# Kernel tuning notes

Hardware: AMD Instinct MI355X
Metric: run time of the kernel (lower is better)

The kernel has to match this reference:

```python
import jax, jax.numpy as jnp
import numpy as np

N_NODES = 100000
N_EDGES = 1600000
IN_CH, HID_CH, N_CLASS = 512, 128, 40


def setup_inputs() -> dict:
    key = jax.random.key(0)
    k1, k2, k3, k4 = jax.random.split(key, 4)
    x = jax.random.normal(k1, (N_NODES, IN_CH), dtype=jnp.float32)
    edge_index = jax.random.randint(k2, (2, N_EDGES), 0, N_NODES, dtype=jnp.int64)
    W1 = jax.random.normal(k3, (IN_CH, HID_CH), dtype=jnp.float32) * (1.0 / np.sqrt(IN_CH))
    b1 = jnp.zeros((HID_CH,), dtype=jnp.float32)
    W2 = jax.random.normal(k4, (HID_CH, N_CLASS), dtype=jnp.float32) * (1.0 / np.sqrt(HID_CH))
    b2 = jnp.zeros((N_CLASS,), dtype=jnp.float32)
    return {"x": x, "edge_index": edge_index, "W1": W1, "b1": b1, "W2": W2, "b2": b2}


def _gcn_conv(x, src, dst, norm, W, b, n_nodes):
    # transform then sparse normalized aggregation: out = D^-1/2 (A+I) D^-1/2 (x W) + b
    h = x @ W                                  # [N, out_ch]
    msg = h[src] * norm[:, None]               # gather + scale, [E+N, out_ch]
    return jax.ops.segment_sum(msg, dst, num_segments=n_nodes) + b


def reference(x, edge_index, W1, b1, W2, b2):
    n = x.shape[0]
    loop = jnp.arange(n, dtype=edge_index.dtype)
    src = jnp.concatenate([edge_index[0], loop])   # add self-loops
    dst = jnp.concatenate([edge_index[1], loop])
    deg = jax.ops.segment_sum(jnp.ones_like(src, dtype=x.dtype), dst, num_segments=n)
    dinv = jnp.where(deg > 0, jax.lax.rsqrt(deg), 0.0)
    norm = dinv[src] * dinv[dst]                   # symmetric normalization

    h = jax.nn.relu(_gcn_conv(x, src, dst, norm, W1, b1, n))
    # dropout(p=0.5, train=False) -> identity in eval mode
    logits = _gcn_conv(h, src, dst, norm, W2, b2, n)
    return jax.nn.log_softmax(logits, axis=1)
```

## Files before the change

kernel.cpp:

```cpp
#include <hip/hip_runtime.h>
#include <math.h>

#define IN_CH 512
#define HID 128
#define NCLASS 40
#define SCAN_CHUNK 2048
#define FILL_CHUNKS 2048

typedef __attribute__((ext_vector_type(8))) short short8;
typedef __attribute__((ext_vector_type(4))) float float4v;

static __device__ inline ushort f2bf(float f) {
    unsigned int u = __float_as_uint(f);
    u += 0x7fffu + ((u >> 16) & 1u);
    return (ushort)(u >> 16);
}
static __device__ inline float bf2f(ushort u) {
    return __uint_as_float(((unsigned int)u) << 16);
}

__global__ void k_count(const int* __restrict__ dst, int E, int* __restrict__ cnt) {
    int i = blockIdx.x * blockDim.x + threadIdx.x;
    if (i < E) atomicAdd(&cnt[dst[i]], 1);
}

__global__ void k_dinv(const int* __restrict__ cnt, float* __restrict__ dinv, int n) {
    int i = blockIdx.x * blockDim.x + threadIdx.x;
    if (i < n) dinv[i] = rsqrtf((float)cnt[i] + 1.0f);
}

__global__ __launch_bounds__(256) void k_scan_local(const int* __restrict__ cnt,
                                                    int* __restrict__ rowptr,
                                                    int* __restrict__ blocksum, int n) {
    __shared__ int ssum[256];
    int b = blockIdx.x, t = threadIdx.x;
    int base = b * SCAN_CHUNK + t * 8;
    int v[8], s = 0;
    #pragma unroll
    for (int i = 0; i < 8; ++i) {
        int idx = base + i;
        v[i] = (idx < n) ? cnt[idx] : 0;
        s += v[i];
    }
    ssum[t] = s;
    __syncthreads();
    for (int off = 1; off < 256; off <<= 1) {
        int x = (t >= off) ? ssum[t - off] : 0;
        __syncthreads();
        ssum[t] += x;
        __syncthreads();
    }
    int run = ssum[t] - s;
    #pragma unroll
    for (int i = 0; i < 8; ++i) {
        int idx = base + i;
        if (idx < n) rowptr[idx] = run;
        run += v[i];
    }
    if (t == 255) blocksum[b] = ssum[255];
}

__global__ void k_scan_blocksums(int* blocksum, int nb) {
    if (threadIdx.x == 0 && blockIdx.x == 0) {
        int acc = 0;
        for (int i = 0; i < nb; ++i) { int v = blocksum[i]; blocksum[i] = acc; acc += v; }
    }
}

__global__ void k_scan_add(int* __restrict__ rowptr, int* __restrict__ cursor,
                           const int* __restrict__ blocksum, int n) {
    int i = blockIdx.x * blockDim.x + threadIdx.x;
    if (i < n) {
        int r = rowptr[i] + blocksum[i / SCAN_CHUNK];
        rowptr[i] = r;
        cursor[i] = r;
    }
}

__global__ __launch_bounds__(256) void k_fill(const int* __restrict__ src,
                                              const int* __restrict__ dst,
                                              int* __restrict__ cursor,
                                              int* __restrict__ col, int E, int N) {
    int range = blockIdx.x & 7;
    int chunk = blockIdx.x >> 3;
    int r0 = (N >> 3) * range;
    int r1 = (range == 7) ? N : r0 + (N >> 3);
    int e0 = (int)((long long)E * chunk / FILL_CHUNKS);
    int e1 = (int)((long long)E * (chunk + 1) / FILL_CHUNKS);
    for (int e = e0 + threadIdx.x; e < e1; e += 256) {
        int d = dst[e];
        if (d >= r0 && d < r1) {
            int p = atomicAdd(&cursor[d], 1);
            col[p] = src[e];
        }
    }
}

__global__ void k_w1t(const float* __restrict__ W1, ushort* __restrict__ W1t) {
    int i = blockIdx.x * blockDim.x + threadIdx.x;
    int n = i >> 9;
    int k = i & 511;
    W1t[i] = f2bf(W1[k * HID + n]);
}

#define GBM 128
#define GBK 64
#define KP 72
__global__ __launch_bounds__(256) void k_gemm1_mfma(const float* __restrict__ X,
                                                    const ushort* __restrict__ W1t,
                                                    ushort* __restrict__ H, int M) {
    __shared__ ushort As[GBM * KP];
    int t = threadIdx.x;
    int bm = blockIdx.x * GBM;
    int wave = t >> 6;
    int lane = t & 63;
    int m0w = (wave >> 1) * 64;
    int n0w = (wave & 1) * 64;
    int lrow = lane & 15;
    int quad = lane >> 4;

    float4v acc[4][4];
    #pragma unroll
    for (int i = 0; i < 4; ++i)
        #pragma unroll
        for (int j = 0; j < 4; ++j) acc[i][j] = (float4v)(0.f);

    int ar = t >> 1;
    int ah = (t & 1) * 32;
    int gmr = bm + ar;
    if (gmr >= M) gmr = M - 1;
    const float* gA = &X[(size_t)gmr * IN_CH + ah];

    float4 pre[8];
    #pragma unroll
    for (int i = 0; i < 8; ++i) pre[i] = *(const float4*)(gA + i * 4);

    for (int k0 = 0; k0 < IN_CH; k0 += GBK) {
        #pragma unroll
        for (int i = 0; i < 4; ++i) {
            union { ushort u[8]; uint4 v; } pk;
            float4 f0 = pre[2 * i], f1 = pre[2 * i + 1];
            pk.u[0] = f2bf(f0.x); pk.u[1] = f2bf(f0.y);
            pk.u[2] = f2bf(f0.z); pk.u[3] = f2bf(f0.w);
            pk.u[4] = f2bf(f1.x); pk.u[5] = f2bf(f1.y);
            pk.u[6] = f2bf(f1.z); pk.u[7] = f2bf(f1.w);
            *(uint4*)&As[ar * KP + ah + i * 8] = pk.v;
        }
        if (k0 + GBK < IN_CH) {
            #pragma unroll
            for (int i = 0; i < 8; ++i)
                pre[i] = *(const float4*)(gA + k0 + GBK + i * 4);
        }
        __syncthreads();
        #pragma unroll
        for (int kk = 0; kk < GBK; kk += 32) {
            short8 af[4], bfr[4];
            #pragma unroll
            for (int j = 0; j < 4; ++j)
                bfr[j] = *(const short8*)&W1t[(size_t)(n0w + j * 16 + lrow) * IN_CH
                                              + k0 + kk + quad * 8];
            #pragma unroll
            for (int i = 0; i < 4; ++i)
                af[i] = *(const short8*)&As[(m0w + i * 16 + lrow) * KP + kk + quad * 8];
            #pragma unroll
            for (int i = 0; i < 4; ++i)
                #pragma unroll
                for (int j = 0; j < 4; ++j)
                    acc[i][j] = __builtin_amdgcn_mfma_f32_16x16x32_bf16(
                        af[i], bfr[j], acc[i][j], 0, 0, 0);
        }
        __syncthreads();
    }
    #pragma unroll
    for (int i = 0; i < 4; ++i) {
        #pragma unroll
        for (int r = 0; r < 4; ++r) {
            int gm = bm + m0w + i * 16 + quad * 4 + r;
            if (gm < M) {
                #pragma unroll
                for (int j = 0; j < 4; ++j)
                    H[(size_t)gm * HID + n0w + j * 16 + lrow] = f2bf(acc[i][j][r]);
            }
        }
    }
}

__global__ __launch_bounds__(256) void k_agg1_gemm2(const int* __restrict__ rowptr,
                                                    const int* __restrict__ rowend,
                                                    const int* __restrict__ col,
                                                    const float* __restrict__ dinv,
                                                    const unsigned int* __restrict__ h1b,
                                                    const float* __restrict__ b1,
                                                    const float* __restrict__ W2,
                                                    unsigned int* __restrict__ h2p, int N) {
    __shared__ float hs[4][HID];
    int wv = threadIdx.x >> 6;
    int t  = threadIdx.x & 63;
    int m = blockIdx.x * 4 + wv;
    if (m >= N) m = N - 1;
    float dm = dinv[m];
    unsigned int sv = h1b[(size_t)m * 64 + t];
    float sw = dm * dm;
    float ax = bf2f((ushort)(sv & 0xffff)) * sw;
    float ay = bf2f((ushort)(sv >> 16)) * sw;
    int j = rowptr[m], jend = rowend[m];
    for (; j + 4 <= jend; j += 4) {
        int s0 = col[j], s1 = col[j + 1], s2 = col[j + 2], s3 = col[j + 3];
        float n0 = dinv[s0] * dm, n1 = dinv[s1] * dm;
        float n2 = dinv[s2] * dm, n3 = dinv[s3] * dm;
        unsigned int v0 = h1b[(size_t)s0 * 64 + t];
        unsigned int v1 = h1b[(size_t)s1 * 64 + t];
        unsigned int v2 = h1b[(size_t)s2 * 64 + t];
        unsigned int v3 = h1b[(size_t)s3 * 64 + t];
        ax += bf2f((ushort)(v0 & 0xffff)) * n0;
        ay += bf2f((ushort)(v0 >> 16)) * n0;
        ax += bf2f((ushort)(v1 & 0xffff)) * n1;
        ay += bf2f((ushort)(v1 >> 16)) * n1;
        ax += bf2f((ushort)(v2 & 0xffff)) * n2;
        ay += bf2f((ushort)(v2 >> 16)) * n2;
        ax += bf2f((ushort)(v3 & 0xffff)) * n3;
        ay += bf2f((ushort)(v3 >> 16)) * n3;
    }
    for (; j < jend; ++j) {
        int s = col[j];
        float nrm = dinv[s] * dm;
        unsigned int v = h1b[(size_t)s * 64 + t];
        ax += bf2f((ushort)(v & 0xffff)) * nrm;
        ay += bf2f((ushort)(v >> 16)) * nrm;
    }
    float2 bb = ((const float2*)b1)[t];
    ax = fmaxf(ax + bb.x, 0.f);
    ay = fmaxf(ay + bb.y, 0.f);
    *(float2*)&hs[wv][2 * t] = make_float2(ax, ay);
    __syncthreads();
    float acc = 0.f;
    if (t < NCLASS) {
        #pragma unroll 8
        for (int k = 0; k < HID; ++k) acc += hs[wv][k] * W2[k * NCLASS + t];
    }
    unsigned int bv = (unsigned int)f2bf(acc);
    unsigned int lo = __shfl(bv, 2 * t);
    unsigned int hi = __shfl(bv, 2 * t + 1);
    if (t < 20) h2p[(size_t)m * 20 + t] = lo | (hi << 16);
}

__global__ __launch_bounds__(256) void k_agg2_final(const int* __restrict__ rowptr,
                                                    const int* __restrict__ rowend,
                                                    const int* __restrict__ col,
                                                    const float* __restrict__ dinv,
                                                    const unsigned int* __restrict__ h2p,
                                                    const float* __restrict__ b2,
                                                    float* __restrict__ out, int N) {
    int wv = threadIdx.x >> 6;
    int t  = threadIdx.x & 63;
    int m = blockIdx.x * 4 + wv;
    if (m >= N) m = N - 1;
    float dm = dinv[m];
    bool act = t < 20;
    float vx = 0.f, vy = 0.f;
    if (act) {
        unsigned int v = h2p[(size_t)m * 20 + t];
        float sw = dm * dm;
        vx = bf2f((ushort)(v & 0xffff)) * sw;
        vy = bf2f((ushort)(v >> 16)) * sw;
    }
    int j = rowptr[m], jend = rowend[m];
    for (; j + 4 <= jend; j += 4) {
        int s0 = col[j], s1 = col[j + 1], s2 = col[j + 2], s3 = col[j + 3];
        float n0 = dinv[s0] * dm, n1 = dinv[s1] * dm;
        float n2 = dinv[s2] * dm, n3 = dinv[s3] * dm;
        if (act) {
            unsigned int v0 = h2p[(size_t)s0 * 20 + t];
            unsigned int v1 = h2p[(size_t)s1 * 20 + t];
            unsigned int v2 = h2p[(size_t)s2 * 20 + t];
            unsigned int v3 = h2p[(size_t)s3 * 20 + t];
            vx += bf2f((ushort)(v0 & 0xffff)) * n0;
            vy += bf2f((ushort)(v0 >> 16)) * n0;
            vx += bf2f((ushort)(v1 & 0xffff)) * n1;
            vy += bf2f((ushort)(v1 >> 16)) * n1;
            vx += bf2f((ushort)(v2 & 0xffff)) * n2;
            vy += bf2f((ushort)(v2 >> 16)) * n2;
            vx += bf2f((ushort)(v3 & 0xffff)) * n3;
            vy += bf2f((ushort)(v3 >> 16)) * n3;
        }
    }
    for (; j < jend; ++j) {
        int s = col[j];
        float nrm = dinv[s] * dm;
        if (act) {
            unsigned int v = h2p[(size_t)s * 20 + t];
            vx += bf2f((ushort)(v & 0xffff)) * nrm;
            vy += bf2f((ushort)(v >> 16)) * nrm;
        }
    }
    if (act) {
        float2 bb = ((const float2*)b2)[t];
        vx += bb.x;
        vy += bb.y;
    }
    float mv = act ? fmaxf(vx, vy) : -INFINITY;
    #pragma unroll
    for (int off = 32; off; off >>= 1) mv = fmaxf(mv, __shfl_xor(mv, off));
    float ex = act ? (expf(vx - mv) + expf(vy - mv)) : 0.f;
    #pragma unroll
    for (int off = 32; off; off >>= 1) ex += __shfl_xor(ex, off);
    float lse = mv + logf(ex);
    if (act) ((float2*)out)[(size_t)m * 20 + t] = make_float2(vx - lse, vy - lse);
}

extern "C" void kernel_launch(void* const* d_in, const int* in_sizes, int n_in,
                              void* d_out, int out_size, void* d_ws, size_t ws_size,
                              hipStream_t stream) {
    const float* x  = (const float*)d_in[0];
    const int*   ei = (const int*)d_in[1];
    const float* W1 = (const float*)d_in[2];
    const float* b1 = (const float*)d_in[3];
    const float* W2 = (const float*)d_in[4];
    const float* b2 = (const float*)d_in[5];
    float* out = (float*)d_out;

    const int N = in_sizes[0] / IN_CH;
    const int E = in_sizes[1] / 2;
    const int* src = ei;
    const int* dst = ei + E;

    const int NB_SCAN = (N + SCAN_CHUNK - 1) / SCAN_CHUNK;

    size_t Npad = ((size_t)N + 127) / 128 * 128;
    float* ws = (float*)d_ws;
    float* dinv    = ws;
    int*   cnt     = (int*)(ws + Npad);
    int*   rowptr  = (int*)(ws + 2 * Npad);
    int*   cursor  = (int*)(ws + 3 * Npad);
    int*   bsum    = (int*)(ws + 4 * Npad);
    int*   col     = (int*)(ws + 4 * Npad + 128);
    size_t o_h1    = 4 * Npad + 128 + (size_t)E;
    unsigned int* h1b = (unsigned int*)(ws + o_h1);
    unsigned int* h2p = (unsigned int*)(ws + o_h1 + (size_t)N * 64);
    ushort* W1t    = (ushort*)h2p;

    hipMemsetAsync(cnt, 0, (size_t)N * sizeof(int), stream);
    k_count<<<(E + 255) / 256, 256, 0, stream>>>(dst, E, cnt);
    k_dinv<<<(N + 255) / 256, 256, 0, stream>>>(cnt, dinv, N);
    k_scan_local<<<NB_SCAN, 256, 0, stream>>>(cnt, rowptr, bsum, N);
    k_scan_blocksums<<<1, 64, 0, stream>>>(bsum, NB_SCAN);
    k_scan_add<<<(N + 255) / 256, 256, 0, stream>>>(rowptr, cursor, bsum, N);
    k_fill<<<8 * FILL_CHUNKS, 256, 0, stream>>>(src, dst, cursor, col, E, N);

    k_w1t<<<(HID * IN_CH) / 256, 256, 0, stream>>>(W1, W1t);
    k_gemm1_mfma<<<(N + GBM - 1) / GBM, 256, 0, stream>>>(x, W1t, (ushort*)h1b, N);
    k_agg1_gemm2<<<(N + 3) / 4, 256, 0, stream>>>(rowptr, cursor, col, dinv,
                                                  h1b, b1, W2, h2p, N);

    k_agg2_final<<<(N + 3) / 4, 256, 0, stream>>>(rowptr, cursor, col, dinv,
                                                  h2p, b2, out, N);
}
```

Measured before the change: 702.7 us.

## Pre-scale features by dinv, split GEMM2 onto MFMA, parallelize agg2 edges

Folds the source-side D^-1/2 into the GEMM1 epilogue and the agg1 output. This removes the per-edge dinv gathers and multiplies in both aggregations. The scalar per-wave layer-2 matmul fused into agg1 becomes a separate bf16 MFMA kernel over a transposed, padded W2. Agg2 now spreads edges over three 20-lane groups and combines them with shuffles, and agg1 uses dual accumulators with 8-way unrolling. The cost is an extra kernel launch and an extra bf16 round trip of the hidden activations through memory.

```diff
diff --git a/kernel.cpp b/kernel.cpp
--- a/kernel.cpp
+++ b/kernel.cpp
@@ -103,11 +103,20 @@
     W1t[i] = f2bf(W1[k * HID + n]);
 }
 
+__global__ void k_w2t(const float* __restrict__ W2, ushort* __restrict__ W2t) {
+    int i = blockIdx.x * blockDim.x + threadIdx.x;
+    int n = i >> 7;
+    int k = i & 127;
+    float v = (n < NCLASS) ? W2[k * NCLASS + n] : 0.f;
+    W2t[i] = f2bf(v);
+}
+
 #define GBM 128
 #define GBK 64
 #define KP 72
 __global__ __launch_bounds__(256) void k_gemm1_mfma(const float* __restrict__ X,
                                                     const ushort* __restrict__ W1t,
+                                                    const float* __restrict__ dinv,
                                                     ushort* __restrict__ H, int M) {
     __shared__ ushort As[GBM * KP];
     int t = threadIdx.x;
@@ -177,71 +186,109 @@
         for (int r = 0; r < 4; ++r) {
             int gm = bm + m0w + i * 16 + quad * 4 + r;
             if (gm < M) {
+                float di = dinv[gm];
                 #pragma unroll
                 for (int j = 0; j < 4; ++j)
-                    H[(size_t)gm * HID + n0w + j * 16 + lrow] = f2bf(acc[i][j][r]);
+                    H[(size_t)gm * HID + n0w + j * 16 + lrow] = f2bf(acc[i][j][r] * di);
             }
         }
     }
 }
 
-__global__ __launch_bounds__(256) void k_agg1_gemm2(const int* __restrict__ rowptr,
-                                                    const int* __restrict__ rowend,
-                                                    const int* __restrict__ col,
-                                                    const float* __restrict__ dinv,
-                                                    const unsigned int* __restrict__ h1b,
-                                                    const float* __restrict__ b1,
-                                                    const float* __restrict__ W2,
-                                                    unsigned int* __restrict__ h2p, int N) {
-    __shared__ float hs[4][HID];
+__global__ __launch_bounds__(256) void k_agg1(const int* __restrict__ rowptr,
+                                              const int* __restrict__ rowend,
+                                              const int* __restrict__ col,
+                                              const float* __restrict__ dinv,
+                                              const unsigned int* __restrict__ h1b,
+                                              const float* __restrict__ b1,
+                                              unsigned int* __restrict__ hb, int N) {
     int wv = threadIdx.x >> 6;
     int t  = threadIdx.x & 63;
     int m = blockIdx.x * 4 + wv;
     if (m >= N) m = N - 1;
     float dm = dinv[m];
     unsigned int sv = h1b[(size_t)m * 64 + t];
-    float sw = dm * dm;
-    float ax = bf2f((ushort)(sv & 0xffff)) * sw;
-    float ay = bf2f((ushort)(sv >> 16)) * sw;
+    float ax = bf2f((ushort)(sv & 0xffff));
+    float ay = bf2f((ushort)(sv >> 16));
+    float bx = 0.f, by = 0.f;
     int j = rowptr[m], jend = rowend[m];
-    for (; j + 4 <= jend; j += 4) {
-        int s0 = col[j], s1 = col[j + 1], s2 = col[j + 2], s3 = col[j + 3];
-        float n0 = dinv[s0] * dm, n1 = dinv[s1] * dm;
-        float n2 = dinv[s2] * dm, n3 = dinv[s3] * dm;
+    for (; j + 8 <= jend; j += 8) {
+        int s0 = col[j],     s1 = col[j + 1], s2 = col[j + 2], s3 = col[j + 3];
+        int s4 = col[j + 4], s5 = col[j + 5], s6 = col[j + 6], s7 = col[j + 7];
         unsigned int v0 = h1b[(size_t)s0 * 64 + t];
         unsigned int v1 = h1b[(size_t)s1 * 64 + t];
         unsigned int v2 = h1b[(size_t)s2 * 64 + t];
         unsigned int v3 = h1b[(size_t)s3 * 64 + t];
-        ax += bf2f((ushort)(v0 & 0xffff)) * n0;
-        ay += bf2f((ushort)(v0 >> 16)) * n0;
-        ax += bf2f((ushort)(v1 & 0xffff)) * n1;
-        ay += bf2f((ushort)(v1 >> 16)) * n1;
-        ax += bf2f((ushort)(v2 & 0xffff)) * n2;
-        ay += bf2f((ushort)(v2 >> 16)) * n2;
-        ax += bf2f((ushort)(v3 & 0xffff)) * n3;
-        ay += bf2f((ushort)(v3 >> 16)) * n3;
+        unsigned int v4 = h1b[(size_t)s4 * 64 + t];
+        unsigned int v5 = h1b[(size_t)s5 * 64 + t];
+        unsigned int v6 = h1b[(size_t)s6 * 64 + t];
+        unsigned int v7 = h1b[(size_t)s7 * 64 + t];
+        ax += bf2f((ushort)(v0 & 0xffff)); ay += bf2f((ushort)(v0 >> 16));
+        bx += bf2f((ushort)(v1 & 0xffff)); by += bf2f((ushort)(v1 >> 16));
+        ax += bf2f((ushort)(v2 & 0xffff)); ay += bf2f((ushort)(v2 >> 16));
+        bx += bf2f((ushort)(v3 & 0xffff)); by += bf2f((ushort)(v3 >> 16));
+        ax += bf2f((ushort)(v4 & 0xffff)); ay += bf2f((ushort)(v4 >> 16));
+        bx += bf2f((ushort)(v5 & 0xffff)); by += bf2f((ushort)(v5 >> 16));
+        ax += bf2f((ushort)(v6 & 0xffff)); ay += bf2f((ushort)(v6 >> 16));
+        bx += bf2f((ushort)(v7 & 0xffff)); by += bf2f((ushort)(v7 >> 16));
+    }
+    for (; j + 4 <= jend; j += 4) {
+        int s0 = col[j], s1 = col[j + 1], s2 = col[j + 2], s3 = col[j + 3];
+        unsigned int v0 = h1b[(size_t)s0 * 64 + t];
+        unsigned int v1 = h1b[(size_t)s1 * 64 + t];
+        unsigned int v2 = h1b[(size_t)s2 * 64 + t];
+        unsigned int v3 = h1b[(size_t)s3 * 64 + t];
+        ax += bf2f((ushort)(v0 & 0xffff)); ay += bf2f((ushort)(v0 >> 16));
+        bx += bf2f((ushort)(v1 & 0xffff)); by += bf2f((ushort)(v1 >> 16));
+        ax += bf2f((ushort)(v2 & 0xffff)); ay += bf2f((ushort)(v2 >> 16));
+        bx += bf2f((ushort)(v3 & 0xffff)); by += bf2f((ushort)(v3 >> 16));
     }
     for (; j < jend; ++j) {
         int s = col[j];
-        float nrm = dinv[s] * dm;
         unsigned int v = h1b[(size_t)s * 64 + t];
-        ax += bf2f((ushort)(v & 0xffff)) * nrm;
-        ay += bf2f((ushort)(v >> 16)) * nrm;
-    }
+        ax += bf2f((ushort)(v & 0xffff)); ay += bf2f((ushort)(v >> 16));
+    }
+    ax += bx; ay += by;
     float2 bb = ((const float2*)b1)[t];
-    ax = fmaxf(ax + bb.x, 0.f);
-    ay = fmaxf(ay + bb.y, 0.f);
-    *(float2*)&hs[wv][2 * t] = make_float2(ax, ay);
-    __syncthreads();
-    float acc = 0.f;
-    if (t < NCLASS) {
-        #pragma unroll 8
-        for (int k = 0; k < HID; ++k) acc += hs[wv][k] * W2[k * NCLASS + t];
-    }
-    unsigned int bv = (unsigned int)f2bf(acc);
-    unsigned int lo = __shfl(bv, 2 * t);
-    unsigned int hi = __shfl(bv, 2 * t + 1);
-    if (t < 20) h2p[(size_t)m * 20 + t] = lo | (hi << 16);
+    float hx = fmaxf(fmaf(ax, dm, bb.x), 0.f);
+    float hy = fmaxf(fmaf(ay, dm, bb.y), 0.f);
+    hx *= dm;
+    hy *= dm;
+    hb[(size_t)m * 64 + t] = (unsigned int)f2bf(hx) | ((unsigned int)f2bf(hy) << 16);
+}
+
+__global__ __launch_bounds__(256) void k_gemm2_mfma(const ushort* __restrict__ hb,
+                                                    const ushort* __restrict__ W2t,
+                                                    ushort* __restrict__ h2s, int M) {
+    int t = threadIdx.x;
+    int wave = t >> 6, lane = t & 63;
+    int lrow = lane & 15, quad = lane >> 4;
+    int row0 = blockIdx.x * 64 + wave * 16;
+    int rm = row0 + lrow;
+    if (rm >= M) rm = M - 1;
+    const ushort* pa = &hb[(size_t)rm * HID + quad * 8];
+    float4v acc[3];
+    acc[0] = (float4v)(0.f); acc[1] = (float4v)(0.f); acc[2] = (float4v)(0.f);
+    #pragma unroll
+    for (int k0 = 0; k0 < HID; k0 += 32) {
+        short8 a = *(const short8*)(pa + k0);
+        #pragma unroll
+        for (int jj = 0; jj < 3; ++jj) {
+            short8 b = *(const short8*)&W2t[(size_t)(jj * 16 + lrow) * HID
+                                            + k0 + quad * 8];
+            acc[jj] = __builtin_amdgcn_mfma_f32_16x16x32_bf16(a, b, acc[jj], 0, 0, 0);
+        }
+    }
+    #pragma unroll
+    for (int jj = 0; jj < 3; ++jj) {
+        int cls = jj * 16 + lrow;
+        #pragma unroll
+        for (int r = 0; r < 4; ++r) {
+            int node = row0 + quad * 4 + r;
+            if (node < M && cls < NCLASS)
+                h2s[(size_t)node * NCLASS + cls] = f2bf(acc[jj][r]);
+        }
+    }
 }
 
 __global__ __launch_bounds__(256) void k_agg2_final(const int* __restrict__ rowptr,
@@ -256,56 +303,47 @@
     int m = blockIdx.x * 4 + wv;
     if (m >= N) m = N - 1;
     float dm = dinv[m];
-    bool act = t < 20;
+    int g = (t >= 40) ? 2 : ((t >= 20) ? 1 : 0);
+    int u = t - g * 20;
+    bool act = t < 60;
     float vx = 0.f, vy = 0.f;
+    if (t < 20) {
+        unsigned int v = h2p[(size_t)m * 20 + u];
+        vx = bf2f((ushort)(v & 0xffff));
+        vy = bf2f((ushort)(v >> 16));
+    }
+    int j = rowptr[m] + g, jend = rowend[m];
     if (act) {
-        unsigned int v = h2p[(size_t)m * 20 + t];
-        float sw = dm * dm;
-        vx = bf2f((ushort)(v & 0xffff)) * sw;
-        vy = bf2f((ushort)(v >> 16)) * sw;
-    }
-    int j = rowptr[m], jend = rowend[m];
-    for (; j + 4 <= jend; j += 4) {
-        int s0 = col[j], s1 = col[j + 1], s2 = col[j + 2], s3 = col[j + 3];
-        float n0 = dinv[s0] * dm, n1 = dinv[s1] * dm;
-        float n2 = dinv[s2] * dm, n3 = dinv[s3] * dm;
-        if (act) {
-            unsigned int v0 = h2p[(size_t)s0 * 20 + t];
-            unsigned int v1 = h2p[(size_t)s1 * 20 + t];
-            unsigned int v2 = h2p[(size_t)s2 * 20 + t];
-            unsigned int v3 = h2p[(size_t)s3 * 20 + t];
-            vx += bf2f((ushort)(v0 & 0xffff)) * n0;
-            vy += bf2f((ushort)(v0 >> 16)) * n0;
-            vx += bf2f((ushort)(v1 & 0xffff)) * n1;
-            vy += bf2f((ushort)(v1 >> 16)) * n1;
-            vx += bf2f((ushort)(v2 & 0xffff)) * n2;
-            vy += bf2f((ushort)(v2 >> 16)) * n2;
-            vx += bf2f((ushort)(v3 & 0xffff)) * n3;
-            vy += bf2f((ushort)(v3 >> 16)) * n3;
-        }
-    }
-    for (; j < jend; ++j) {
-        int s = col[j];
-        float nrm = dinv[s] * dm;
-        if (act) {
-            unsigned int v = h2p[(size_t)s * 20 + t];
-            vx += bf2f((ushort)(v & 0xffff)) * nrm;
-            vy += bf2f((ushort)(v >> 16)) * nrm;
-        }
-    }
-    if (act) {
-        float2 bb = ((const float2*)b2)[t];
-        vx += bb.x;
-        vy += bb.y;
-    }
-    float mv = act ? fmaxf(vx, vy) : -INFINITY;
+        for (; j + 3 < jend; j += 6) {
+            int s0 = col[j], s1 = col[j + 3];
+            unsigned int v0 = h2p[(size_t)s0 * 20 + u];
+            unsigned int v1 = h2p[(size_t)s1 * 20 + u];
+            vx += bf2f((ushort)(v0 & 0xffff)); vy += bf2f((ushort)(v0 >> 16));
+            vx += bf2f((ushort)(v1 & 0xffff)); vy += bf2f((ushort)(v1 >> 16));
+        }
+        if (j < jend) {
+            int s = col[j];
+            unsigned int v = h2p[(size_t)s * 20 + u];
+            vx += bf2f((ushort)(v & 0xffff)); vy += bf2f((ushort)(v >> 16));
+        }
+    }
+    vx += __shfl(vx, t + 20) + __shfl(vx, t + 40);
+    vy += __shfl(vy, t + 20) + __shfl(vy, t + 40);
+    bool w = t < 20;
+    float lx = 0.f, ly = 0.f;
+    if (w) {
+        float2 bb = ((const float2*)b2)[u];
+        lx = fmaf(vx, dm, bb.x);
+        ly = fmaf(vy, dm, bb.y);
+    }
+    float mv = w ? fmaxf(lx, ly) : -INFINITY;
     #pragma unroll
     for (int off = 32; off; off >>= 1) mv = fmaxf(mv, __shfl_xor(mv, off));
-    float ex = act ? (expf(vx - mv) + expf(vy - mv)) : 0.f;
+    float ex = w ? (expf(lx - mv) + expf(ly - mv)) : 0.f;
     #pragma unroll
     for (int off = 32; off; off >>= 1) ex += __shfl_xor(ex, off);
     float lse = mv + logf(ex);
-    if (act) ((float2*)out)[(size_t)m * 20 + t] = make_float2(vx - lse, vy - lse);
+    if (w) ((float2*)out)[(size_t)m * 20 + u] = make_float2(lx - lse, ly - lse);
 }
 
 extern "C" void kernel_launch(void* const* d_in, const int* in_sizes, int n_in,
@@ -336,8 +374,10 @@
     int*   col     = (int*)(ws + 4 * Npad + 128);
     size_t o_h1    = 4 * Npad + 128 + (size_t)E;
     unsigned int* h1b = (unsigned int*)(ws + o_h1);
-    unsigned int* h2p = (unsigned int*)(ws + o_h1 + (size_t)N * 64);
-    ushort* W1t    = (ushort*)h2p;
+    unsigned int* hb  = (unsigned int*)(ws + o_h1 + (size_t)N * 64);
+    unsigned int* h2p = (unsigned int*)(ws + o_h1 + (size_t)N * 128);
+    ushort* W2t = (ushort*)(ws + o_h1 + (size_t)N * 148);
+    ushort* W1t = (ushort*)h2p;
 
     hipMemsetAsync(cnt, 0, (size_t)N * sizeof(int), stream);
     k_count<<<(E + 255) / 256, 256, 0, stream>>>(dst, E, cnt);
@@ -348,10 +388,14 @@
     k_fill<<<8 * FILL_CHUNKS, 256, 0, stream>>>(src, dst, cursor, col, E, N);
 
     k_w1t<<<(HID * IN_CH) / 256, 256, 0, stream>>>(W1, W1t);
-    k_gemm1_mfma<<<(N + GBM - 1) / GBM, 256, 0, stream>>>(x, W1t, (ushort*)h1b, N);
-    k_agg1_gemm2<<<(N + 3) / 4, 256, 0, stream>>>(rowptr, cursor, col, dinv,
-                                                  h1b, b1, W2, h2p, N);
-
+    k_w2t<<<24, 256, 0, stream>>>(W2, W2t);
+    k_gemm1_mfma<<<(N + GBM - 1) / GBM, 256, 0, stream>>>(x, W1t, dinv,
+                                                          (ushort*)h1b, N);
+    k_agg1<<<(N + 3) / 4, 256, 0, stream>>>(rowptr, cursor, col, dinv,
+                                            h1b, b1, hb, N);
+
+    k_gemm2_mfma<<<(N + 63) / 64, 256, 0, stream>>>((const ushort*)hb, W2t,
+                                                    (ushort*)h2p, N);
     k_agg2_final<<<(N + 3) / 4, 256, 0, stream>>>(rowptr, cursor, col, dinv,
                                                   h2p, b2, out, N);
 }
```

Result: faster. 616.7 us (-12.2%).
